# Optimization experiments

Measured on AMD Instinct MI355X. Metric: run time of the kernel, lower is better.

Reference implementation:

```python
import jax, jax.numpy as jnp
import numpy as np

E = 8        # num_expert
D = 768      # d_model
H = 3072     # expert hidden = 4*d_model
K = 2        # top_k
N = 4096     # tokens
C = 2048


def setup_inputs() -> dict:
    key = jax.random.key(0)
    k0, k1, k2, k3 = jax.random.split(key, 4)
    moe_inp = jax.random.normal(k0, (N, D), dtype=jnp.float32)
    gate_w = jax.random.normal(k1, (D, E), dtype=jnp.float32) / np.sqrt(D).astype(np.float32)
    gate_b = jnp.zeros((E,), dtype=jnp.float32)
    w1 = jax.random.normal(k2, (E, D, H), dtype=jnp.float32) / np.sqrt(D).astype(np.float32)
    b1 = jnp.zeros((E, H), dtype=jnp.float32)
    w2 = jax.random.normal(k3, (E, H, D), dtype=jnp.float32) / np.sqrt(H).astype(np.float32)
    b2 = jnp.zeros((E, D), dtype=jnp.float32)
    return {"moe_inp": moe_inp, "gate_w": gate_w, "gate_b": gate_b,
            "w1": w1, "b1": b1, "w2": w2, "b2": b2}


def reference(moe_inp, gate_w, gate_b, w1, b1, w2, b2):
    # --- NaiveGate: linear scores, top-k experts, softmax over the k scores ---
    logits = moe_inp @ gate_w + gate_b                      # [N, E]
    top_v, top_i = jax.lax.top_k(logits, K)                 # [N, K]
    gate_score = jax.nn.softmax(top_v, axis=-1)             # [N, K]

    # --- scatter tokens to expert-contiguous capacity buffers (MOEScatter) ---
    flat_e = top_i.reshape(-1)                              # [N*K] expert id per slot
    onehot = jax.nn.one_hot(flat_e, E, dtype=jnp.int32)     # [N*K, E]
    # running position of each token inside its expert's buffer
    pos = jnp.sum(jnp.cumsum(onehot, axis=0) * onehot, axis=1) - 1  # [N*K]
    x_rep = jnp.repeat(moe_inp, K, axis=0)                  # [N*K, D]
    xe = jnp.zeros((E, C, D), dtype=moe_inp.dtype).at[flat_e, pos].set(x_rep, mode='drop')

    # --- grouped expert FFN (expert_fn): per-expert batched GEMMs ---
    h = jax.nn.gelu(jnp.einsum('ecd,edh->ech', xe, w1) + b1[:, None, :])
    ye = jnp.einsum('ech,ehd->ecd', h, w2) + b2[:, None, :]  # [E, C, D]

    # --- gather back to token order (MOEGather) and combine with gate scores ---
    y_flat = ye.at[flat_e, pos].get(mode='fill', fill_value=0.0)  # [N*K, D]
    out = jnp.einsum('nkd,nk->nd', y_flat.reshape(N, K, D), gate_score)
    return out
```

## Files before the change

kernel.cpp:

```cpp
#include <hip/hip_runtime.h>
#include <hip/hip_bf16.h>
#include <math.h>

#define NT    4096
#define DM    768
#define HD    3072
#define NE    8
#define CAP   2048
#define SLOTS_MAX 9216
#define WDIM1 72
#define BINCAP1 9
#define WDIM2 40
#define BINCAP2 5

typedef __attribute__((ext_vector_type(8))) short bf16x8;
typedef __attribute__((ext_vector_type(4))) float f32x4;

__device__ __forceinline__ unsigned short f2bf(float f) {
  unsigned int u = __float_as_uint(f);
  unsigned int r = (u + 0x7fffu + ((u >> 16) & 1u)) >> 16;
  return (unsigned short)r;
}

__device__ __forceinline__ void async16(const unsigned short* g, unsigned short* l) {
  __builtin_amdgcn_global_load_lds((const __attribute__((address_space(1))) void*)g,
                                   (__attribute__((address_space(3))) void*)l,
                                   16, 0, 0);
}

__global__ void convert_x_kernel(const float* __restrict__ x,
                                 unsigned short* __restrict__ xb) {
  int i = (blockIdx.x * 256 + threadIdx.x) * 4;
  float4 v = *(const float4*)(x + i);
  uint2 o;
  o.x = (unsigned int)f2bf(v.x) | ((unsigned int)f2bf(v.y) << 16);
  o.y = (unsigned int)f2bf(v.z) | ((unsigned int)f2bf(v.w) << 16);
  *(uint2*)(xb + i) = o;
}

__global__ __launch_bounds__(256) void transpose_kernel(
    const float* __restrict__ src, unsigned short* __restrict__ dst,
    int R, int src_stride, int col_off,
    size_t src_e_stride, size_t dst_e_stride, int ncx) {
  __shared__ unsigned int tile32[64 * 129];
  const int b = blockIdx.x;
  const int e = b & 7;
  const int idx = b >> 3;
  const int c0 = (idx % ncx) * 64;
  const int r0 = (idx / ncx) * 256;
  const float* s = src + (size_t)e * src_e_stride + col_off;
  unsigned short* d = dst + (size_t)e * dst_e_stride;
  const int t = threadIdx.x;
  const int q16 = t & 15;
  const int tg = t >> 4;
#pragma unroll
  for (int i = 0; i < 8; i++) {
    int rl = tg * 2 + i * 32;
    const float4 f0 = *(const float4*)(s + (size_t)(r0 + rl) * src_stride + c0 + q16 * 4);
    const float4 f1 = *(const float4*)(s + (size_t)(r0 + rl + 1) * src_stride + c0 + q16 * 4);
    int j = tg + i * 16;
    tile32[(q16 * 4 + 0) * 129 + j] = (unsigned int)f2bf(f0.x) | ((unsigned int)f2bf(f1.x) << 16);
    tile32[(q16 * 4 + 1) * 129 + j] = (unsigned int)f2bf(f0.y) | ((unsigned int)f2bf(f1.y) << 16);
    tile32[(q16 * 4 + 2) * 129 + j] = (unsigned int)f2bf(f0.z) | ((unsigned int)f2bf(f1.z) << 16);
    tile32[(q16 * 4 + 3) * 129 + j] = (unsigned int)f2bf(f0.w) | ((unsigned int)f2bf(f1.w) << 16);
  }
  __syncthreads();
#pragma unroll
  for (int i = 0; i < 4; i++) {
    int cl = tg + i * 16;
    unsigned short* drow = d + (size_t)(c0 + cl) * R + r0;
#pragma unroll
    for (int half = 0; half < 2; half++) {
      int u = q16 * 4 + half * 64;
      uint4 v;
      v.x = tile32[cl * 129 + u + 0];
      v.y = tile32[cl * 129 + u + 1];
      v.z = tile32[cl * 129 + u + 2];
      v.w = tile32[cl * 129 + u + 3];
      *(uint4*)(drow + q16 * 8 + half * 128) = v;
    }
  }
}

__global__ void gate_dots_kernel(const float* __restrict__ inp,
                                 const float* __restrict__ gw,
                                 const float* __restrict__ gb,
                                 int2* __restrict__ tope,
                                 float2* __restrict__ tops) {
  const int tok  = blockIdx.x * 4 + (threadIdx.x >> 6);
  const int lane = threadIdx.x & 63;
  const float* x = inp + (size_t)tok * DM;
  float acc[NE];
#pragma unroll
  for (int e = 0; e < NE; e++) acc[e] = 0.f;
  for (int d = lane; d < DM; d += 64) {
    float xv = x[d];
    const float4 w0 = *(const float4*)(gw + d * NE);
    const float4 w1v = *(const float4*)(gw + d * NE + 4);
    acc[0] += xv * w0.x; acc[1] += xv * w0.y;
    acc[2] += xv * w0.z; acc[3] += xv * w0.w;
    acc[4] += xv * w1v.x; acc[5] += xv * w1v.y;
    acc[6] += xv * w1v.z; acc[7] += xv * w1v.w;
  }
#pragma unroll
  for (int e = 0; e < NE; e++) {
    float v = acc[e];
#pragma unroll
    for (int m = 32; m > 0; m >>= 1) v += __shfl_xor(v, m, 64);
    acc[e] = v + gb[e];
  }
  if (lane == 0) {
    float bv = -1e30f, sv = -1e30f; int bi = 0, si = 0;
#pragma unroll
    for (int e = 0; e < NE; e++) {
      float v = acc[e];
      if (v > bv)      { sv = bv; si = bi; bv = v; bi = e; }
      else if (v > sv) { sv = v;  si = e; }
    }
    float e1 = expf(sv - bv);
    float s0 = 1.f / (1.f + e1);
    float s1 = e1 / (1.f + e1);
    tope[tok] = make_int2(bi, si);
    tops[tok] = make_float2(s0, s1);
  }
}

__device__ __forceinline__ int agg_inc(int* lcnt, int key) {
  const int lane = threadIdx.x & 63;
  int p = 0;
#pragma unroll
  for (int ee = 0; ee < NE; ee++) {
    unsigned long long m = __ballot(key == ee);
    if (m) {
      int leader = __ffsll(m) - 1;
      int n = __popcll(m);
      int b = 0;
      if (lane == leader) b = atomicAdd(&lcnt[ee], n);
      b = __shfl(b, leader, 64);
      if (key == ee) p = b + __popcll(m & ((1ull << lane) - 1ull));
    }
  }
  return p;
}

__global__ void assign_kernel(const int2* __restrict__ tope,
                              int* __restrict__ cnt,
                              int* __restrict__ base,
                              int* __restrict__ src,
                              int2* __restrict__ pos,
                              int2* __restrict__ wl1,
                              int2* __restrict__ wl2) {
  __shared__ int lcnt[NE];
  const int t = threadIdx.x;
  if (t < NE) lcnt[t] = 0;
  __syncthreads();
  for (int i = t; i < NT; i += 1024) {
    int2 e = tope[i];
    int p0 = agg_inc(lcnt, e.x);
    int p1 = agg_inc(lcnt, e.y);
    if (p0 < CAP) src[e.x * CAP + p0] = i;
    if (p1 < CAP) src[e.y * CAP + p1] = i;
    pos[i] = make_int2(p0, p1);
  }
  __syncthreads();
  if (t == 0) {
    int b = 0;
    for (int e = 0; e < NE; e++) {
      int c = min(lcnt[e], CAP);
      cnt[e] = c;
      base[e] = b;
      b += (c + 127) & ~127;
    }
    for (int s = 0; s < WDIM1; s++) wl1[s] = make_int2(-1, 0);
    int bin = 0, fill = 0;
    for (int e = 0; e < NE; e++) {
      int ntl = (cnt[e] + 127) >> 7;
      for (int mt = 0; mt < ntl; mt++) {
        if (fill == BINCAP1) { bin++; fill = 0; }
        wl1[fill * 8 + bin] = make_int2(e, mt * 128);
        fill++;
      }
    }
    for (int s = 0; s < WDIM2; s++) wl2[s] = make_int2(-1, 0);
    bin = 0; fill = 0;
    for (int e = 0; e < NE; e++) {
      int ntl = (cnt[e] + 255) >> 8;
      for (int mt = 0; mt < ntl; mt++) {
        if (fill == BINCAP2) { bin++; fill = 0; }
        wl2[fill * 8 + bin] = make_int2(e, mt * 256);
        fill++;
      }
    }
  }
}

__global__ __launch_bounds__(256) void gemm1_kernel(
    const unsigned short* __restrict__ xb,
    const unsigned short* __restrict__ w1t,
    const float* __restrict__ b1,
    const int* __restrict__ cnt,
    const int* __restrict__ base,
    const int* __restrict__ src,
    const int2* __restrict__ wl,
    unsigned short* __restrict__ h,
    int hoff, int chunk) {
  const int b = blockIdx.x;
  const int wi = b % WDIM1;
  const int nt = b / WDIM1;
  const int2 wle = wl[wi];
  if (wle.x < 0) return;
  const int e = wle.x;
  const int m0 = wle.y;
  const int n0 = nt * 128;
  const int count = cnt[e];
  const int hb = base[e];

  __shared__ unsigned short As[3 * 4096];
  __shared__ unsigned short Bs[3 * 4096];

  const int t = threadIdx.x;
  const int lane = t & 63;
  const int wave = t >> 6;
  const int r0 = t >> 2;
  const int kc = ((t & 3) ^ ((t >> 3) & 3)) * 8;

  const int tok0 = (m0 + r0      < count) ? src[e * CAP + m0 + r0]      : 0;
  const int tok1 = (m0 + r0 + 64 < count) ? src[e * CAP + m0 + r0 + 64] : 0;
  const unsigned short* aptr0 = xb + (size_t)tok0 * DM + kc;
  const unsigned short* aptr1 = xb + (size_t)tok1 * DM + kc;
  const unsigned short* w1e = w1t + (size_t)e * chunk * DM;
  const unsigned short* bptr0 = w1e + (size_t)(n0 + r0) * DM + kc;
  const unsigned short* bptr1 = bptr0 + (size_t)64 * DM;

  const int wrow = (wave >> 1) * 64;
  const int wcol = (wave & 1) * 64;
  const int lrow = lane & 15;
  const int koff = ((lane >> 4) ^ ((lane >> 1) & 3)) * 8;

  f32x4 acc[4][4];
#pragma unroll
  for (int i = 0; i < 4; i++)
#pragma unroll
    for (int j = 0; j < 4; j++) acc[i][j] = (f32x4){0.f, 0.f, 0.f, 0.f};

#define STAGE1(bi, kk) do {                                   \
    unsigned short* A_ = As + (bi) * 4096 + wave * 512;       \
    unsigned short* B_ = Bs + (bi) * 4096 + wave * 512;       \
    async16(aptr0 + (kk), A_);                                \
    async16(aptr1 + (kk), A_ + 2048);                         \
    async16(bptr0 + (kk), B_);                                \
    async16(bptr1 + (kk), B_ + 2048);                         \
  } while (0)

#define COMPUTE1(bi) do {                                               \
    const unsigned short* A_ = As + (bi) * 4096;                        \
    const unsigned short* B_ = Bs + (bi) * 4096;                        \
    bf16x8 af[4], bfr[4];                                               \
    _Pragma("unroll")                                                   \
    for (int i = 0; i < 4; i++)                                         \
      af[i] = *(const bf16x8*)(A_ + (wrow + i * 16 + lrow) * 32 + koff);\
    _Pragma("unroll")                                                   \
    for (int j = 0; j < 4; j++)                                         \
      bfr[j] = *(const bf16x8*)(B_ + (wcol + j * 16 + lrow) * 32 + koff);\
    _Pragma("unroll")                                                   \
    for (int i = 0; i < 4; i++)                                         \
      _Pragma("unroll")                                                 \
      for (int j = 0; j < 4; j++)                                       \
        acc[i][j] = __builtin_amdgcn_mfma_f32_16x16x32_bf16(af[i], bfr[j], acc[i][j], 0, 0, 0); \
  } while (0)

  const int NS = DM / 32;
  STAGE1(0, 0);
  STAGE1(1, 32);
  int cur = 0;
  for (int ts = 0; ts < NS - 2; ++ts) {
    int pf = cur + 2; if (pf >= 3) pf -= 3;
    STAGE1(pf, (ts + 2) * 32);
    asm volatile("s_waitcnt vmcnt(8)" ::: "memory");
    __builtin_amdgcn_s_barrier();
    COMPUTE1(cur);
    asm volatile("s_waitcnt lgkmcnt(0)" ::: "memory");
    __builtin_amdgcn_s_barrier();
    if (++cur == 3) cur = 0;
  }
  asm volatile("s_waitcnt vmcnt(4)" ::: "memory");
  __builtin_amdgcn_s_barrier();
  COMPUTE1(cur);
  if (++cur == 3) cur = 0;
  asm volatile("s_waitcnt vmcnt(0)" ::: "memory");
  __builtin_amdgcn_s_barrier();
  COMPUTE1(cur);

  __syncthreads();
  const int q4 = (lane >> 4) * 4;
  const int c = lane & 15;
  unsigned short* slab = (wave < 2) ? (As + wave * 4608) : (Bs + (wave - 2) * 4608);
#pragma unroll
  for (int j = 0; j < 4; j++) {
    const float bias = b1[e * HD + hoff + n0 + wcol + j * 16 + c];
#pragma unroll
    for (int i = 0; i < 4; i++) {
#pragma unroll
      for (int r = 0; r < 4; r++) {
        float v = acc[i][j][r] + bias;
        float u2 = 1.5957691216f * (v + 0.044715f * v * v * v);
        float g = v / (1.f + __expf(-u2));
        slab[(i * 16 + q4 + r) * 72 + j * 16 + c] = f2bf(g);
      }
    }
  }
  asm volatile("s_waitcnt lgkmcnt(0)" ::: "memory");
  const int l8 = lane & 7;
  const int r8 = lane >> 3;
  unsigned short* hrow = h + (size_t)(hb + m0 + wrow) * chunk + n0 + wcol;
#pragma unroll
  for (int p = 0; p < 8; p++) {
    int lm = p * 8 + r8;
    uint4 v = *(const uint4*)(slab + lm * 72 + l8 * 8);
    *(uint4*)(hrow + (size_t)lm * chunk + l8 * 8) = v;
  }
#undef STAGE1
#undef COMPUTE1
}

__global__ __launch_bounds__(512) void gemm2_kernel(
    const unsigned short* __restrict__ h,
    const unsigned short* __restrict__ w2t,
    const int* __restrict__ cnt,
    const int* __restrict__ base,
    const int2* __restrict__ wl,
    float* __restrict__ ye,
    int chunk, int add_prev) {
  const int b = blockIdx.x;
  const int wi = b % WDIM2;
  const int fast = b / WDIM2;
  const int2 wle = wl[wi];
  if (wle.x < 0) return;
  const int e = wle.x;
  const int m0 = wle.y;
  const int kh = fast / 3;
  const int n0 = (fast % 3) * 256;
  const int count = cnt[e];
  const int cpad = (count + 127) & ~127;
  const int hb = base[e];
  const int khalf = chunk >> 1;

  __shared__ unsigned short As[3 * 8192];
  __shared__ unsigned short Bs[3 * 8192];

  const int t = threadIdx.x;
  const int lane = t & 63;
  const int wave = t >> 6;
  const int r0 = t >> 2;
  const int kc = ((t & 3) ^ ((t >> 3) & 3)) * 8;

  const unsigned short* aptr0 = h + (size_t)(hb + m0 + r0) * chunk + kh * khalf + kc;
  const unsigned short* aptr1 = aptr0 + (size_t)128 * chunk;
  const unsigned short* w2e = w2t + (size_t)e * DM * chunk;
  const unsigned short* bptr0 = w2e + (size_t)(n0 + r0) * chunk + kh * khalf + kc;
  const unsigned short* bptr1 = bptr0 + (size_t)128 * chunk;

  const int wrow = (wave >> 2) * 128;
  const int wcol = (wave & 3) * 64;
  const int lrow = lane & 15;
  const int koff = ((lane >> 4) ^ ((lane >> 1) & 3)) * 8;

  f32x4 acc[8][4];
#pragma unroll
  for (int i = 0; i < 8; i++)
#pragma unroll
    for (int j = 0; j < 4; j++) acc[i][j] = (f32x4){0.f, 0.f, 0.f, 0.f};

#define STAGE2(bi, kk) do {                                   \
    unsigned short* A_ = As + (bi) * 8192 + wave * 512;       \
    unsigned short* B_ = Bs + (bi) * 8192 + wave * 512;       \
    async16(aptr0 + (kk), A_);                                \
    async16(aptr1 + (kk), A_ + 4096);                         \
    async16(bptr0 + (kk), B_);                                \
    async16(bptr1 + (kk), B_ + 4096);                         \
  } while (0)

#define COMPUTE2(bi) do {                                               \
    const unsigned short* A_ = As + (bi) * 8192;                        \
    const unsigned short* B_ = Bs + (bi) * 8192;                        \
    bf16x8 af[8], bfr[4];                                               \
    _Pragma("unroll")                                                   \
    for (int i = 0; i < 8; i++)                                         \
      af[i] = *(const bf16x8*)(A_ + (wrow + i * 16 + lrow) * 32 + koff);\
    _Pragma("unroll")                                                   \
    for (int j = 0; j < 4; j++)                                         \
      bfr[j] = *(const bf16x8*)(B_ + (wcol + j * 16 + lrow) * 32 + koff);\
    _Pragma("unroll")                                                   \
    for (int i = 0; i < 8; i++)                                         \
      _Pragma("unroll")                                                 \
      for (int j = 0; j < 4; j++)                                       \
        acc[i][j] = __builtin_amdgcn_mfma_f32_16x16x32_bf16(af[i], bfr[j], acc[i][j], 0, 0, 0); \
  } while (0)

  const int NS = khalf >> 5;
  STAGE2(0, 0);
  STAGE2(1, 32);
  int cur = 0;
  for (int ts = 0; ts < NS - 2; ++ts) {
    int pf = cur + 2; if (pf >= 3) pf -= 3;
    STAGE2(pf, (ts + 2) * 32);
    asm volatile("s_waitcnt vmcnt(8)" ::: "memory");
    __builtin_amdgcn_s_barrier();
    COMPUTE2(cur);
    asm volatile("s_waitcnt lgkmcnt(0)" ::: "memory");
    __builtin_amdgcn_s_barrier();
    if (++cur == 3) cur = 0;
  }
  asm volatile("s_waitcnt vmcnt(4)" ::: "memory");
  __builtin_amdgcn_s_barrier();
  COMPUTE2(cur);
  if (++cur == 3) cur = 0;
  asm volatile("s_waitcnt vmcnt(0)" ::: "memory");
  __builtin_amdgcn_s_barrier();
  COMPUTE2(cur);

  const int q4 = (lane >> 4) * 4;
  const int c = lane & 15;
  float* yrow = ye + (size_t)kh * SLOTS_MAX * DM + (size_t)(hb + m0) * DM + n0;
#pragma unroll
  for (int i = 0; i < 8; i++) {
#pragma unroll
    for (int r = 0; r < 4; r++) {
      int m = wrow + i * 16 + q4 + r;
      if (m0 + m < cpad) {
#pragma unroll
        for (int j = 0; j < 4; j++) {
          int n = wcol + j * 16 + c;
          float v = acc[i][j][r];
          if (add_prev) v += yrow[(size_t)m * DM + n];
          yrow[(size_t)m * DM + n] = v;
        }
      }
    }
  }
#undef STAGE2
#undef COMPUTE2
}

__global__ void gather_kernel(const float* __restrict__ ye,
                              const float* __restrict__ b2,
                              const int2* __restrict__ tope,
                              const float2* __restrict__ tops,
                              const int2* __restrict__ pos,
                              const int* __restrict__ base,
                              float* __restrict__ out) {
  int idx = blockIdx.x * 256 + threadIdx.x;
  int tok = idx / (DM / 4);
  int d4 = (idx % (DM / 4)) * 4;
  int2 e = tope[tok];
  float2 s = tops[tok];
  int2 p = pos[tok];
  const float* ye1 = ye + (size_t)SLOTS_MAX * DM;
  float4 r = make_float4(0.f, 0.f, 0.f, 0.f);
  if (p.x < CAP) {
    size_t row = (size_t)(base[e.x] + p.x) * DM + d4;
    const float4 va = *(const float4*)(ye + row);
    const float4 vb = *(const float4*)(ye1 + row);
    const float4 bb = *(const float4*)(b2 + e.x * DM + d4);
    r.x += s.x * (va.x + vb.x + bb.x); r.y += s.x * (va.y + vb.y + bb.y);
    r.z += s.x * (va.z + vb.z + bb.z); r.w += s.x * (va.w + vb.w + bb.w);
  }
  if (p.y < CAP) {
    size_t row = (size_t)(base[e.y] + p.y) * DM + d4;
    const float4 va = *(const float4*)(ye + row);
    const float4 vb = *(const float4*)(ye1 + row);
    const float4 bb = *(const float4*)(b2 + e.y * DM + d4);
    r.x += s.y * (va.x + vb.x + bb.x); r.y += s.y * (va.y + vb.y + bb.y);
    r.z += s.y * (va.z + vb.z + bb.z); r.w += s.y * (va.w + vb.w + bb.w);
  }
  *(float4*)(out + (size_t)tok * DM + d4) = r;
}

extern "C" void kernel_launch(void* const* d_in, const int* in_sizes, int n_in,
                              void* d_out, int out_size, void* d_ws, size_t ws_size,
                              hipStream_t stream) {
  const float* inp = (const float*)d_in[0];
  const float* gw  = (const float*)d_in[1];
  const float* gb  = (const float*)d_in[2];
  const float* w1  = (const float*)d_in[3];
  const float* b1  = (const float*)d_in[4];
  const float* w2  = (const float*)d_in[5];
  const float* b2  = (const float*)d_in[6];
  float* out = (float*)d_out;

  const size_t meta = 165376;
  const int cands[6] = {3072, 1536, 1024, 768, 512, 256};
  int chunk = 256;
  for (int ci = 0; ci < 6; ci++) {
    int c = cands[ci];
    size_t need = meta + (size_t)NT * DM * 2
                + (size_t)NE * c * DM * 2
                + (size_t)SLOTS_MAX * c * 2
                + 2 * (size_t)SLOTS_MAX * DM * 4;
    if (need <= ws_size) { chunk = c; break; }
  }

  char* ws = (char*)d_ws;
  int*    cnt  = (int*)(ws);
  int*    base = (int*)(ws + 256);
  int*    srcb = (int*)(ws + 512);
  int2*   tope = (int2*)(ws + 66048);
  float2* tops = (float2*)(ws + 98816);
  int2*   pos  = (int2*)(ws + 131584);
  int2*   wl1  = (int2*)(ws + 164352);
  int2*   wl2  = (int2*)(ws + 164928);
  size_t off = meta;
  unsigned short* xb = (unsigned short*)(ws + off);  off += (size_t)NT * DM * 2;
  unsigned short* wt = (unsigned short*)(ws + off);  off += (size_t)NE * chunk * DM * 2;
  unsigned short* hc = (unsigned short*)(ws + off);  off += (size_t)SLOTS_MAX * chunk * 2;
  float* ye = (float*)(ws + off);

  convert_x_kernel<<<(NT * DM) / 1024, 256, 0, stream>>>(inp, xb);
  gate_dots_kernel<<<NT / 4, 256, 0, stream>>>(inp, gw, gb, tope, tops);
  assign_kernel<<<1, 1024, 0, stream>>>(tope, cnt, base, srcb, pos, wl1, wl2);

  for (int c = 0; c < HD; c += chunk) {
    transpose_kernel<<<NE * (chunk / 64) * (DM / 256), 256, 0, stream>>>(
        w1, wt, DM, HD, c, (size_t)DM * HD, (size_t)chunk * DM, chunk / 64);
    gemm1_kernel<<<(chunk / 128) * WDIM1, 256, 0, stream>>>(
        xb, wt, b1, cnt, base, srcb, wl1, hc, c, chunk);
    transpose_kernel<<<NE * (DM / 64) * (chunk / 256), 256, 0, stream>>>(
        w2 + (size_t)c * DM, wt, chunk, DM, 0, (size_t)HD * DM, (size_t)DM * chunk, DM / 64);
    gemm2_kernel<<<(2 * DM / 256) * WDIM2, 512, 0, stream>>>(
        hc, wt, cnt, base, wl2, ye, chunk, c == 0 ? 0 : 1);
  }

  gather_kernel<<<(NT * DM / 4) / 256, 256, 0, stream>>>(ye, b2, tope, tops, pos, base, out);
}
```

Before: 382.0 us.

## Fuse prep kernels and both weight transposes into combined launches

Merges the x-to-bf16 conversion, the gate/top-k computation and the first chunk's w1/w2 transposes into a single block-partitioned prep kernel. Later chunks run both transposes in one launch. Separate w1t and w2t buffers replace the shared one, so the two GEMMs no longer serialize on a single scratch buffer. This removes several kernel launches and gives each launch more blocks to run concurrently. The cost is extra workspace, which may force a smaller chunk size if the workspace is tight.

```diff
diff --git a/kernel.cpp b/kernel.cpp
--- a/kernel.cpp
+++ b/kernel.cpp
@@ -28,26 +28,15 @@
                                    16, 0, 0);
 }
 
-__global__ void convert_x_kernel(const float* __restrict__ x,
-                                 unsigned short* __restrict__ xb) {
-  int i = (blockIdx.x * 256 + threadIdx.x) * 4;
-  float4 v = *(const float4*)(x + i);
-  uint2 o;
-  o.x = (unsigned int)f2bf(v.x) | ((unsigned int)f2bf(v.y) << 16);
-  o.y = (unsigned int)f2bf(v.z) | ((unsigned int)f2bf(v.w) << 16);
-  *(uint2*)(xb + i) = o;
-}
-
-__global__ __launch_bounds__(256) void transpose_kernel(
-    const float* __restrict__ src, unsigned short* __restrict__ dst,
+__device__ __forceinline__ void transpose_body(
+    int idx, const float* __restrict__ src, unsigned short* __restrict__ dst,
     int R, int src_stride, int col_off,
-    size_t src_e_stride, size_t dst_e_stride, int ncx) {
-  __shared__ unsigned int tile32[64 * 129];
-  const int b = blockIdx.x;
-  const int e = b & 7;
-  const int idx = b >> 3;
-  const int c0 = (idx % ncx) * 64;
-  const int r0 = (idx / ncx) * 256;
+    size_t src_e_stride, size_t dst_e_stride, int ncx,
+    unsigned int* tile32) {
+  const int e = idx & 7;
+  const int rest = idx >> 3;
+  const int c0 = (rest % ncx) * 64;
+  const int r0 = (rest / ncx) * 256;
   const float* s = src + (size_t)e * src_e_stride + col_off;
   unsigned short* d = dst + (size_t)e * dst_e_stride;
   const int t = threadIdx.x;
@@ -82,46 +71,78 @@
   }
 }
 
-__global__ void gate_dots_kernel(const float* __restrict__ inp,
-                                 const float* __restrict__ gw,
-                                 const float* __restrict__ gb,
-                                 int2* __restrict__ tope,
-                                 float2* __restrict__ tops) {
-  const int tok  = blockIdx.x * 4 + (threadIdx.x >> 6);
-  const int lane = threadIdx.x & 63;
-  const float* x = inp + (size_t)tok * DM;
-  float acc[NE];
-#pragma unroll
-  for (int e = 0; e < NE; e++) acc[e] = 0.f;
-  for (int d = lane; d < DM; d += 64) {
-    float xv = x[d];
-    const float4 w0 = *(const float4*)(gw + d * NE);
-    const float4 w1v = *(const float4*)(gw + d * NE + 4);
-    acc[0] += xv * w0.x; acc[1] += xv * w0.y;
-    acc[2] += xv * w0.z; acc[3] += xv * w0.w;
-    acc[4] += xv * w1v.x; acc[5] += xv * w1v.y;
-    acc[6] += xv * w1v.z; acc[7] += xv * w1v.w;
-  }
-#pragma unroll
-  for (int e = 0; e < NE; e++) {
-    float v = acc[e];
-#pragma unroll
-    for (int m = 32; m > 0; m >>= 1) v += __shfl_xor(v, m, 64);
-    acc[e] = v + gb[e];
-  }
-  if (lane == 0) {
-    float bv = -1e30f, sv = -1e30f; int bi = 0, si = 0;
+__global__ __launch_bounds__(256) void prep_kernel(
+    const float* __restrict__ inp, unsigned short* __restrict__ xb,
+    const float* __restrict__ gw, const float* __restrict__ gb,
+    int2* __restrict__ tope, float2* __restrict__ tops,
+    const float* __restrict__ w1, unsigned short* __restrict__ w1t,
+    const float* __restrict__ w2, unsigned short* __restrict__ w2t,
+    int chunk, int nconv, int ngate, int nt1, int nt2) {
+  __shared__ unsigned int tile32[64 * 129];
+  const int b = blockIdx.x;
+  if (b < nconv) {
+    int i = (b * 256 + threadIdx.x) * 4;
+    float4 v = *(const float4*)(inp + i);
+    uint2 o;
+    o.x = (unsigned int)f2bf(v.x) | ((unsigned int)f2bf(v.y) << 16);
+    o.y = (unsigned int)f2bf(v.z) | ((unsigned int)f2bf(v.w) << 16);
+    *(uint2*)(xb + i) = o;
+  } else if (b < nconv + ngate) {
+    const int tok  = (b - nconv) * 4 + (threadIdx.x >> 6);
+    const int lane = threadIdx.x & 63;
+    const float* x = inp + (size_t)tok * DM;
+    float acc[NE];
+#pragma unroll
+    for (int e = 0; e < NE; e++) acc[e] = 0.f;
+    for (int d = lane; d < DM; d += 64) {
+      float xv = x[d];
+      const float4 w0 = *(const float4*)(gw + d * NE);
+      const float4 w1v = *(const float4*)(gw + d * NE + 4);
+      acc[0] += xv * w0.x; acc[1] += xv * w0.y;
+      acc[2] += xv * w0.z; acc[3] += xv * w0.w;
+      acc[4] += xv * w1v.x; acc[5] += xv * w1v.y;
+      acc[6] += xv * w1v.z; acc[7] += xv * w1v.w;
+    }
 #pragma unroll
     for (int e = 0; e < NE; e++) {
       float v = acc[e];
-      if (v > bv)      { sv = bv; si = bi; bv = v; bi = e; }
-      else if (v > sv) { sv = v;  si = e; }
-    }
-    float e1 = expf(sv - bv);
-    float s0 = 1.f / (1.f + e1);
-    float s1 = e1 / (1.f + e1);
-    tope[tok] = make_int2(bi, si);
-    tops[tok] = make_float2(s0, s1);
+#pragma unroll
+      for (int m = 32; m > 0; m >>= 1) v += __shfl_xor(v, m, 64);
+      acc[e] = v + gb[e];
+    }
+    if (lane == 0) {
+      float bv = -1e30f, sv = -1e30f; int bi = 0, si = 0;
+#pragma unroll
+      for (int e = 0; e < NE; e++) {
+        float v = acc[e];
+        if (v > bv)      { sv = bv; si = bi; bv = v; bi = e; }
+        else if (v > sv) { sv = v;  si = e; }
+      }
+      float e1 = expf(sv - bv);
+      tope[tok] = make_int2(bi, si);
+      tops[tok] = make_float2(1.f / (1.f + e1), e1 / (1.f + e1));
+    }
+  } else if (b < nconv + ngate + nt1) {
+    transpose_body(b - nconv - ngate, w1, w1t, DM, HD, 0,
+                   (size_t)DM * HD, (size_t)chunk * DM, chunk / 64, tile32);
+  } else {
+    transpose_body(b - nconv - ngate - nt1, w2, w2t, chunk, DM, 0,
+                   (size_t)HD * DM, (size_t)DM * chunk, DM / 64, tile32);
+  }
+}
+
+__global__ __launch_bounds__(256) void transpose_both_kernel(
+    const float* __restrict__ w1, unsigned short* __restrict__ w1t,
+    const float* __restrict__ w2, unsigned short* __restrict__ w2t,
+    int chunk, int c, int nt1) {
+  __shared__ unsigned int tile32[64 * 129];
+  const int b = blockIdx.x;
+  if (b < nt1) {
+    transpose_body(b, w1, w1t, DM, HD, c,
+                   (size_t)DM * HD, (size_t)chunk * DM, chunk / 64, tile32);
+  } else {
+    transpose_body(b - nt1, w2 + (size_t)c * DM, w2t, chunk, DM, 0,
+                   (size_t)HD * DM, (size_t)DM * chunk, DM / 64, tile32);
   }
 }
 
@@ -494,7 +515,7 @@
   for (int ci = 0; ci < 6; ci++) {
     int c = cands[ci];
     size_t need = meta + (size_t)NT * DM * 2
-                + (size_t)NE * c * DM * 2
+                + 2 * (size_t)NE * c * DM * 2
                 + (size_t)SLOTS_MAX * c * 2
                 + 2 * (size_t)SLOTS_MAX * DM * 4;
     if (need <= ws_size) { chunk = c; break; }
@@ -510,24 +531,30 @@
   int2*   wl1  = (int2*)(ws + 164352);
   int2*   wl2  = (int2*)(ws + 164928);
   size_t off = meta;
-  unsigned short* xb = (unsigned short*)(ws + off);  off += (size_t)NT * DM * 2;
-  unsigned short* wt = (unsigned short*)(ws + off);  off += (size_t)NE * chunk * DM * 2;
-  unsigned short* hc = (unsigned short*)(ws + off);  off += (size_t)SLOTS_MAX * chunk * 2;
+  unsigned short* xb  = (unsigned short*)(ws + off);  off += (size_t)NT * DM * 2;
+  unsigned short* w1t = (unsigned short*)(ws + off);  off += (size_t)NE * chunk * DM * 2;
+  unsigned short* w2t = (unsigned short*)(ws + off);  off += (size_t)NE * chunk * DM * 2;
+  unsigned short* hc  = (unsigned short*)(ws + off);  off += (size_t)SLOTS_MAX * chunk * 2;
   float* ye = (float*)(ws + off);
 
-  convert_x_kernel<<<(NT * DM) / 1024, 256, 0, stream>>>(inp, xb);
-  gate_dots_kernel<<<NT / 4, 256, 0, stream>>>(inp, gw, gb, tope, tops);
+  const int nconv = (NT * DM) / 1024;
+  const int ngate = NT / 4;
+  const int nt1 = NE * (chunk / 64) * (DM / 256);
+  const int nt2 = NE * (DM / 64) * (chunk / 256);
+
+  prep_kernel<<<nconv + ngate + nt1 + nt2, 256, 0, stream>>>(
+      inp, xb, gw, gb, tope, tops, w1, w1t, w2, w2t,
+      chunk, nconv, ngate, nt1, nt2);
   assign_kernel<<<1, 1024, 0, stream>>>(tope, cnt, base, srcb, pos, wl1, wl2);
 
   for (int c = 0; c < HD; c += chunk) {
-    transpose_kernel<<<NE * (chunk / 64) * (DM / 256), 256, 0, stream>>>(
-        w1, wt, DM, HD, c, (size_t)DM * HD, (size_t)chunk * DM, chunk / 64);
+    if (c > 0)
+      transpose_both_kernel<<<nt1 + nt2, 256, 0, stream>>>(
+          w1, w1t, w2, w2t, chunk, c, nt1);
     gemm1_kernel<<<(chunk / 128) * WDIM1, 256, 0, stream>>>(
-        xb, wt, b1, cnt, base, srcb, wl1, hc, c, chunk);
-    transpose_kernel<<<NE * (DM / 64) * (chunk / 256), 256, 0, stream>>>(
-        w2 + (size_t)c * DM, wt, chunk, DM, 0, (size_t)HD * DM, (size_t)DM * chunk, DM / 64);
+        xb, w1t, b1, cnt, base, srcb, wl1, hc, c, chunk);
     gemm2_kernel<<<(2 * DM / 256) * WDIM2, 512, 0, stream>>>(
-        hc, wt, cnt, base, wl2, ye, chunk, c == 0 ? 0 : 1);
+        hc, w2t, cnt, base, wl2, ye, chunk, c == 0 ? 0 : 1);
   }
 
   gather_kernel<<<(NT * DM / 4) / 256, 256, 0, stream>>>(ye, b2, tope, tops, pos, base, out);
```

Measured after the change: 372.9 us. 1.02x faster.
